# Optimization experiments

Hardware: AMD Instinct MI355X
Metric: run time of the kernel (lower is better)

Reference implementation:

```python
import jax, jax.numpy as jnp
import numpy as np

N = 50000          # n_sample
F = 64             # n_feature
DEG = 16           # edges per node
E = N * DEG
HID = 256          # n_hidden
NCLS = 16          # n_class
NPOOL = 3
K = 2              # propagation steps
ALPHA = 1.0        # Propagation alpha
EPS = 1e-5
NODE_POOL = round(N ** (1.0 / NPOOL))          # 37
N0 = round(N / NODE_POOL)                      # 1351
N1 = round(N0 / NODE_POOL)                     # 37
N2 = round(N1 / NODE_POOL)                     # 1


def setup_inputs():
    key = jax.random.key(0)
    ks = jax.random.split(key, 16)
    x = jax.random.normal(ks[0], (N, F), jnp.float32)
    x_cov = jax.random.uniform(ks[1], (N, F), jnp.float32)
    adj_rows = jnp.asarray(np.repeat(np.arange(N, dtype=np.int32), DEG))  # sorted
    adj_cols = jax.random.randint(ks[2], (E,), 0, N, jnp.int32)
    adj_vals = jax.random.uniform(ks[3], (E,), jnp.float32)
    feature_corr = jax.random.uniform(ks[4], (N2, F), jnp.float32)
    bn_gamma = jnp.ones((F,), jnp.float32)
    bn_beta = jnp.zeros((F,), jnp.float32)
    lin = lambda k, i, o: jax.random.normal(k, (i, o), jnp.float32) * 0.05
    W0 = lin(ks[5], F, HID); C0 = jax.random.normal(ks[6], (N0, HID), jnp.float32) * 0.05
    W1 = lin(ks[7], F, HID); C1 = jax.random.normal(ks[8], (N1, HID), jnp.float32) * 0.05
    W2 = lin(ks[9], F, HID); C2 = jax.random.normal(ks[10], (N2, HID), jnp.float32) * 0.05
    mW1 = lin(ks[11], 2 * F, HID); mb1 = jnp.zeros((HID,), jnp.float32)
    mp1 = jnp.full((1,), 0.25, jnp.float32)
    mW2 = lin(ks[12], HID, HID); mb2 = jnp.zeros((HID,), jnp.float32)
    mp2 = jnp.full((1,), 0.25, jnp.float32)
    mW3 = lin(ks[13], HID, NCLS); mb3 = jnp.zeros((NCLS,), jnp.float32)
    return dict(x=x, x_cov=x_cov, adj_vals=adj_vals, feature_corr=feature_corr,
                bn_gamma=bn_gamma, bn_beta=bn_beta, W0=W0, C0=C0, W1=W1, C1=C1,
                W2=W2, C2=C2, mW1=mW1, mb1=mb1, mp1=mp1, mW2=mW2, mb2=mb2, mp2=mp2,
                mW3=mW3, mb3=mb3, adj_rows=adj_rows, adj_cols=adj_cols)


def _pool(xc, W, C, nc):
    # ClusteringLayer: project, hard-assign to nearest centroid, mean-pool,
    # corr = per-node squared deviation from its cluster mean (input resolution).
    h = xc @ W                                                    # [n_prev, HID]
    d = (h * h).sum(-1, keepdims=True) - 2.0 * (h @ C.T) + (C * C).sum(-1)[None, :]
    a = jnp.argmin(d, axis=1)                                     # [n_prev] cluster ids
    cnt = jax.ops.segment_sum(jnp.ones((xc.shape[0],), xc.dtype), a, num_segments=nc)
    pooled = jax.ops.segment_sum(xc, a, num_segments=nc) / jnp.maximum(cnt, 1.0)[:, None]
    corr = (xc - pooled[a]) ** 2                                  # [n_prev, F]
    return pooled, corr, a


def _forward(x, x_cov, adj_vals, feature_corr, bn_gamma, bn_beta, W0, C0, W1, C1,
             W2, C2, mW1, mb1, mp1, mW2, mb2, mp2, mW3, mb3, adj_rows, adj_cols):
    # BatchNorm1d (batch statistics)
    mu = x.mean(0)
    var = x.var(0)
    x = (x - mu) / jnp.sqrt(var + EPS) * bn_gamma + bn_beta
    x0 = x
    # pooling hierarchy
    p0, corr0, a0 = _pool(x_cov, W0, C0, N0)
    p1, corr1, a1 = _pool(p0, W1, C1, N1)
    p2, corr2, a2 = _pool(p1, W2, C2, N2)
    loss = (corr1.mean(0) + corr2.mean(0)).mean() / (NPOOL - 1)
    # gains: spmm(hard assignment, corr_next) is a gather
    g0 = 2.0 * jax.nn.sigmoid(corr2[a1] - corr1)          # [N0, F]
    g1 = 2.0 * jax.nn.sigmoid(feature_corr[a2] - corr2)   # [N1, F]
    # composed node->level cluster ids (masks[1] = masks[0] @ masks[1])
    cl0 = a0               # [N]
    cl1 = a1[a0]           # [N]
    r, c = adj_rows, adj_cols
    # (M diag(g) M^T)[r,c] = g[cl(r)]^2 * 1[cl(r)==cl(c)], masked to adj pattern
    same0 = (cl0[r] == cl0[c])[:, None]
    same1 = (cl1[r] == cl1[c])[:, None]
    vals = adj_vals[:, None] \
        + jnp.where(same0, (g0 * g0)[cl0[r]], jnp.float32(0)) \
        + jnp.where(same1, (g1 * g1)[cl1[r]], jnp.float32(0))     # [E, F]
    # per-feature sparse row softmax
    m = jax.ops.segment_max(vals, r, num_segments=N)
    ev = jnp.exp(vals - m[r])
    s = jax.ops.segment_sum(ev, r, num_segments=N)
    A = ev / s[r]                                                  # [E, F]
    # k propagation steps: per-feature spmm + alpha * x0 residual
    for _ in range(K):
        x = jax.ops.segment_sum(A * x[c], r, num_segments=N) + ALPHA * x0
    # MLP head with PReLU, log-probabilities
    h = jnp.concatenate([x, x0], axis=1)
    h = h @ mW1 + mb1
    h = jnp.where(h >= 0, h, mp1 * h)
    h = h @ mW2 + mb2
    h = jnp.where(h >= 0, h, mp2 * h)
    logits = h @ mW3 + mb3
    out = jax.nn.log_softmax(logits, axis=1)
    return out, loss


def reference(x, x_cov, adj_vals, feature_corr, bn_gamma, bn_beta, W0, C0, W1, C1,
              W2, C2, mW1, mb1, mp1, mW2, mb2, mp2, mW3, mb3, adj_rows, adj_cols):
    return _forward(x, x_cov, adj_vals, feature_corr, bn_gamma, bn_beta, W0, C0,
                    W1, C1, W2, C2, mW1, mb1, mp1, mW2, mb2, mp2, mW3, mb3,
                    adj_rows, adj_cols)
```

## Files before the change

kernel.cpp:

```cpp
#include <hip/hip_runtime.h>
#include <math.h>

#define N_NODES 50000
#define FEA 64
#define DEG 16
#define HID 256
#define NCLS 16
#define NP0 1351
#define NP0T 1408
#define CTILES 11
#define NP1 37
#define EPSV 1e-5f

__global__ __launch_bounds__(256) void bn_reduce(const float* __restrict__ x,
                                                 float* __restrict__ bnsum, float* __restrict__ bnsq) {
    __shared__ float s1[256], s2[256];
    int tid = threadIdx.x;
    int f = tid & 63, sub = tid >> 6;
    float a = 0.f, b = 0.f;
    for (int r = blockIdx.x * 4 + sub; r < N_NODES; r += gridDim.x * 4) {
        float v = x[r * FEA + f];
        a += v; b += v * v;
    }
    s1[tid] = a; s2[tid] = b;
    __syncthreads();
    if (tid < 64) {
        a = s1[tid] + s1[tid + 64] + s1[tid + 128] + s1[tid + 192];
        b = s2[tid] + s2[tid + 64] + s2[tid + 128] + s2[tid + 192];
        atomicAdd(&bnsum[tid], a);
        atomicAdd(&bnsq[tid], b);
    }
}

__global__ __launch_bounds__(256) void bn_apply(const float* __restrict__ x,
                                                const float* __restrict__ bnsum, const float* __restrict__ bnsq,
                                                const float* __restrict__ gamma, const float* __restrict__ beta,
                                                float* __restrict__ x0) {
    int gid = blockIdx.x * 256 + threadIdx.x;
    if (gid >= N_NODES * FEA) return;
    int f = gid & 63;
    float mu = bnsum[f] * (1.0f / N_NODES);
    float var = bnsq[f] * (1.0f / N_NODES) - mu * mu;
    float sc = gamma[f] / sqrtf(var + EPSV);
    x0[gid] = (x[gid] - mu) * sc + beta[f];
}

__global__ void transpose_W0(const float* __restrict__ W0, float* __restrict__ W0t) {
    int idx = blockIdx.x * 256 + threadIdx.x;
    if (idx < FEA * HID) {
        int f = idx >> 8, h = idx & 255;
        W0t[h * FEA + f] = W0[idx];
    }
}

__global__ __launch_bounds__(64) void compute_G2(const float* __restrict__ W0t, const float* __restrict__ C0,
                                                 float* __restrict__ Gt, float* __restrict__ c0n) {
    int j = blockIdx.x, k = threadIdx.x;
    if (j >= NP0) {
        Gt[k * NP0T + j] = 0.f;
        if (k == 0) c0n[j] = 3.4e38f;
        return;
    }
    const float* c = C0 + j * HID;
    float acc = 0.f;
    for (int m = 0; m < HID; ++m) acc += W0t[m * FEA + k] * c[m];
    Gt[k * NP0T + j] = acc;
    float cn = 0.f;
    for (int m = k; m < HID; m += 64) { float v = c[m]; cn += v * v; }
    for (int off = 32; off; off >>= 1) cn += __shfl_xor(cn, off);
    if (k == 0) c0n[j] = cn;
}

__global__ void cnorm(const float* __restrict__ C, float* __restrict__ cn) {
    int j = blockIdx.x, k = threadIdx.x;
    const float* c = C + j * HID;
    float acc = 0.f;
    for (int m = k; m < HID; m += 64) { float v = c[m]; acc += v * v; }
    for (int off = 32; off; off >>= 1) acc += __shfl_xor(acc, off);
    if (k == 0) cn[j] = acc;
}

__global__ __launch_bounds__(256, 2) void argmin0_gemm8(const float* __restrict__ xcov,
                                                        const float* __restrict__ Gt,
                                                        const float* __restrict__ c0n,
                                                        int* __restrict__ a0) {
    __shared__ char smem[36864 + 33792 + 512];
    float* As = (float*)smem;
    float* Bs = (float*)(smem + 36864);
    float* cs = (float*)(smem + 36864 + 33792);
    int t = threadIdx.x;
    int row0 = blockIdx.x * 128;

    {
        int r = t & 127, half = t >> 7;
        int row = row0 + r;
        int fr = r + 4 * (r >> 5);
        if (row < N_NODES) {
            const float4* xp = (const float4*)(xcov + (size_t)row * FEA + half * 32);
            #pragma unroll
            for (int u = 0; u < 8; ++u) {
                float4 v = xp[u];
                int k = half * 32 + u * 4;
                As[(k+0)*144 + fr] = v.x; As[(k+1)*144 + fr] = v.y;
                As[(k+2)*144 + fr] = v.z; As[(k+3)*144 + fr] = v.w;
            }
        } else {
            #pragma unroll
            for (int u = 0; u < 8; ++u) {
                int k = half * 32 + u * 4;
                As[(k+0)*144+fr] = 0.f; As[(k+1)*144+fr] = 0.f;
                As[(k+2)*144+fr] = 0.f; As[(k+3)*144+fr] = 0.f;
            }
        }
    }

    int tr = t & 15, tc = t >> 4;
    int aoff = 8 * tr + 4 * (tr >> 2);
    int boff = 8 * tc;
    unsigned long long best[8];
    #pragma unroll
    for (int r = 0; r < 8; ++r) best[r] = ~0ull;

    for (int tile = 0; tile < CTILES; ++tile) {
        int j0 = tile * 128;
        __syncthreads();
        {
            int kk = t >> 2, g = t & 3;
            const float* gr = Gt + (size_t)kk * NP0T + j0;
            #pragma unroll
            for (int u = 0; u < 8; ++u) {
                int gi = g + 4 * u;
                float4 v = *(const float4*)(gr + gi * 4);
                *(float4*)(Bs + kk * 132 + gi * 4) = v;
            }
        }
        if (t < 128) cs[t] = c0n[j0 + t];
        __syncthreads();

        float acc[8][8];
        #pragma unroll
        for (int r = 0; r < 8; ++r)
            #pragma unroll
            for (int c = 0; c < 8; ++c) acc[r][c] = 0.f;

        for (int k = 0; k < 64; ++k) {
            float4 av0 = *(const float4*)(As + k * 144 + aoff);
            float4 av1 = *(const float4*)(As + k * 144 + aoff + 4);
            float4 bv0 = *(const float4*)(Bs + k * 132 + boff);
            float4 bv1 = *(const float4*)(Bs + k * 132 + boff + 4);
            float av[8] = {av0.x, av0.y, av0.z, av0.w, av1.x, av1.y, av1.z, av1.w};
            float bv[8] = {bv0.x, bv0.y, bv0.z, bv0.w, bv1.x, bv1.y, bv1.z, bv1.w};
            #pragma unroll
            for (int r = 0; r < 8; ++r)
                #pragma unroll
                for (int c = 0; c < 8; ++c) acc[r][c] += av[r] * bv[c];
        }
        #pragma unroll
        for (int c = 0; c < 8; ++c) {
            int j = j0 + boff + c;
            float cn = cs[boff + c];
            #pragma unroll
            for (int r = 0; r < 8; ++r) {
                float d = cn - 2.0f * acc[r][c];
                unsigned s = __float_as_uint(d);
                unsigned u2 = ((int)s < 0) ? ~s : (s | 0x80000000u);
                unsigned long long p = ((unsigned long long)u2 << 32) | (unsigned)j;
                if (p < best[r]) best[r] = p;
            }
        }
    }

    __syncthreads();
    unsigned long long* pmin = (unsigned long long*)Bs;
    #pragma unroll
    for (int r = 0; r < 8; ++r) pmin[(8 * tr + r) * 16 + tc] = best[r];
    __syncthreads();
    if (t < 128) {
        unsigned long long b = pmin[t * 16];
        #pragma unroll
        for (int q = 1; q < 16; ++q) {
            unsigned long long v = pmin[t * 16 + q];
            if (v < b) b = v;
        }
        int row = row0 + t;
        if (row < N_NODES) a0[row] = (int)(unsigned)b;
    }
}

__global__ __launch_bounds__(256) void hist0(const int* __restrict__ a0, int* __restrict__ hist) {
    int i = blockIdx.x * 256 + threadIdx.x;
    bool act = i < N_NODES;
    int j = act ? a0[i] : -1;
    unsigned long long todo = __ballot(act);
    int lane = threadIdx.x & 63;
    while (todo) {
        int leader = __ffsll((long long)todo) - 1;
        int lj = __shfl(j, leader);
        unsigned long long grp = __ballot(act && j == lj);
        if (lane == leader) atomicAdd(&hist[lj], __popcll(grp));
        todo &= ~grp;
    }
}

__global__ __launch_bounds__(256) void scan0(const int* __restrict__ hist, int* __restrict__ off,
                                             int* __restrict__ cursor) {
    __shared__ int wsum[4];
    int t = threadIdx.x;
    int c0 = t * 6;
    int loc[6]; int s = 0;
    #pragma unroll
    for (int u = 0; u < 6; ++u) {
        int j = c0 + u;
        int h = (j < NP0) ? hist[j] : 0;
        loc[u] = s; s += h;
    }
    int lane = t & 63, w = t >> 6;
    int v = s;
    #pragma unroll
    for (int d = 1; d < 64; d <<= 1) {
        int up = __shfl_up(v, d);
        if (lane >= d) v += up;
    }
    if (lane == 63) wsum[w] = v;
    __syncthreads();
    int woff = 0;
    for (int q = 0; q < w; ++q) woff += wsum[q];
    int excl = woff + v - s;
    #pragma unroll
    for (int u = 0; u < 6; ++u) {
        int j = c0 + u;
        if (j < NP0) { off[j] = excl + loc[u]; cursor[j] = excl + loc[u]; }
    }
    if (t == 255) off[NP0] = excl + s;
}

__global__ __launch_bounds__(256) void scatter0(const int* __restrict__ a0, int* __restrict__ cursor,
                                                int* __restrict__ order, int* __restrict__ csrt) {
    int i = blockIdx.x * 256 + threadIdx.x;
    bool act = i < N_NODES;
    int j = act ? a0[i] : -1;
    int lane = threadIdx.x & 63;
    unsigned long long todo = __ballot(act);
    int pos = 0;
    while (todo) {
        int leader = __ffsll((long long)todo) - 1;
        int lj = __shfl(j, leader);
        unsigned long long grp = __ballot(act && j == lj);
        int base = 0;
        if (lane == leader) base = atomicAdd(&cursor[lj], __popcll(grp));
        base = __shfl(base, leader);
        if (act && j == lj)
            pos = base + __popcll(grp & ((1ull << lane) - 1ull));
        todo &= ~grp;
    }
    if (act) { order[pos] = i; csrt[pos] = j; }
}

__global__ __launch_bounds__(256) void pool0seg(const int* __restrict__ order, const int* __restrict__ csrt,
                                                const float* __restrict__ xcov, double* __restrict__ p0d) {
    int lane = threadIdx.x & 63;
    int w = threadIdx.x >> 6;
    int base = (blockIdx.x * 4 + w) * 16;
    if (base >= N_NODES) return;
    int n = N_NODES - base; if (n > 16) n = 16;
    float vals[16]; int cl[16];
    #pragma unroll
    for (int r = 0; r < 16; ++r) {
        if (r < n) {
            int idx = order[base + r];
            cl[r] = csrt[base + r];
            vals[r] = xcov[(size_t)idx * FEA + lane];
        } else { cl[r] = -1; vals[r] = 0.f; }
    }
    double acc = (double)vals[0]; int cur = cl[0];
    #pragma unroll
    for (int r = 1; r < 16; ++r) {
        if (r < n) {
            if (cl[r] == cur) { acc += (double)vals[r]; }
            else { atomicAdd(&p0d[(size_t)cur * FEA + lane], acc); acc = (double)vals[r]; cur = cl[r]; }
        }
    }
    atomicAdd(&p0d[(size_t)cur * FEA + lane], acc);
}

__global__ void pool_fin0(const double* __restrict__ p0d, const int* __restrict__ hist,
                          float* __restrict__ p0, int total) {
    int gid = blockIdx.x * 256 + threadIdx.x;
    if (gid < total) p0[gid] = (float)(p0d[gid] / (double)max(hist[gid >> 6], 1));
}

__global__ __launch_bounds__(64) void level1(const float* __restrict__ p0, const float* __restrict__ W1,
                                             const float* __restrict__ C1, const float* __restrict__ c1n,
                                             int* __restrict__ a1) {
    int i = blockIdx.x;
    int lane = threadIdx.x;
    const float* pr = p0 + (size_t)i * FEA;
    float h[4] = {0.f, 0.f, 0.f, 0.f};
    for (int k = 0; k < FEA; ++k) {
        float pv = pr[k];
        #pragma unroll
        for (int q = 0; q < 4; ++q) h[q] += pv * W1[k * HID + q * 64 + lane];
    }
    float hh = h[0]*h[0] + h[1]*h[1] + h[2]*h[2] + h[3]*h[3];
    for (int off = 32; off; off >>= 1) hh += __shfl_xor(hh, off);
    float best = 3.4e38f; int bj = 0;
    for (int j = 0; j < NP1; ++j) {
        const float* cj = C1 + j * HID;
        float dp = h[0]*cj[lane] + h[1]*cj[64+lane] + h[2]*cj[128+lane] + h[3]*cj[192+lane];
        for (int off = 32; off; off >>= 1) dp += __shfl_xor(dp, off);
        float d = hh - 2.0f * dp + c1n[j];
        if (d < best) { best = d; bj = j; }
    }
    if (lane == 0) a1[i] = bj;
}

__global__ __launch_bounds__(256) void pool1(const float* __restrict__ p0, const int* __restrict__ a1,
                                             float* __restrict__ p1) {
    __shared__ float s[4][64];
    __shared__ int scnt[4];
    int j = blockIdx.x;
    int lane = threadIdx.x & 63, w = threadIdx.x >> 6;
    float acc = 0.f; int cnt = 0;
    for (int i = w; i < NP0; i += 4) {
        if (a1[i] == j) { acc += p0[i * FEA + lane]; cnt++; }
    }
    s[w][lane] = acc;
    if (lane == 0) scnt[w] = cnt;
    __syncthreads();
    if (w == 0) {
        float tsum = s[0][lane] + s[1][lane] + s[2][lane] + s[3][lane];
        int c = scnt[0] + scnt[1] + scnt[2] + scnt[3];
        p1[j * FEA + lane] = tsum / fmaxf((float)c, 1.0f);
    }
}

__global__ __launch_bounds__(256) void level2(const float* __restrict__ p1, const float* __restrict__ fc,
                                              float* __restrict__ corr2, float* __restrict__ g1sq,
                                              float* __restrict__ loss2f) {
    __shared__ float p2s[64];
    __shared__ float lacc[64];
    int tid = threadIdx.x;
    if (tid < 64) {
        float s = 0.f;
        for (int i = 0; i < NP1; ++i) s += p1[i * FEA + tid];
        p2s[tid] = s * (1.0f / NP1);
        lacc[tid] = 0.f;
    }
    __syncthreads();
    for (int t = tid; t < NP1 * FEA; t += 256) {
        int f = t & 63;
        float dv = p1[t] - p2s[f];
        float c2 = dv * dv;
        corr2[t] = c2;
        float sg = 2.0f / (1.0f + __expf(-(fc[f] - c2)));
        g1sq[t] = sg * sg;
        atomicAdd(&lacc[f], c2);
    }
    __syncthreads();
    if (tid < 64) loss2f[tid] = lacc[tid] * (1.0f / NP1);
}

__global__ __launch_bounds__(256) void corr1_g0(const float* __restrict__ p0, const float* __restrict__ p1,
                                                const int* __restrict__ a1, const float* __restrict__ corr2,
                                                float* __restrict__ g0sq, float* __restrict__ loss1g) {
    __shared__ float sh[256];
    int tid = threadIdx.x;
    int f = tid & 63, sub = tid >> 6;
    int i = blockIdx.x * 4 + sub;
    float c1v = 0.f;
    if (i < NP0) {
        int a = a1[i];
        float dv = p0[i * FEA + f] - p1[a * FEA + f];
        c1v = dv * dv;
        float sg = 2.0f / (1.0f + __expf(-(corr2[a * FEA + f] - c1v)));
        g0sq[i * FEA + f] = sg * sg;
    }
    sh[tid] = c1v;
    __syncthreads();
    if (tid < 64) atomicAdd(&loss1g[tid], sh[tid] + sh[tid+64] + sh[tid+128] + sh[tid+192]);
}

__global__ void loss_final(const float* __restrict__ loss1g, const float* __restrict__ loss2f,
                           float* __restrict__ out_loss) {
    int lane = threadIdx.x;
    float v = loss1g[lane] * (1.0f / NP0) + loss2f[lane];
    for (int off = 32; off; off >>= 1) v += __shfl_xor(v, off);
    if (lane == 0) out_loss[0] = v * (1.0f / FEA) * 0.5f;
}

__global__ void cl1map(const int* __restrict__ a0, const int* __restrict__ a1, int* __restrict__ cl1) {
    int i = blockIdx.x * 256 + threadIdx.x;
    if (i < N_NODES) cl1[i] = a1[a0[i]];
}

__global__ __launch_bounds__(256) void prop(const float* __restrict__ xin, const float* __restrict__ x0,
                                            const int* __restrict__ cols, const float* __restrict__ avals,
                                            const int* __restrict__ cl0, const int* __restrict__ cl1,
                                            const float* __restrict__ g0sq, const float* __restrict__ g1sq,
                                            float* __restrict__ xout) {
    int lane = threadIdx.x & 63;
    int i = blockIdx.x * 4 + __builtin_amdgcn_readfirstlane(threadIdx.x >> 6);
    int s0 = cl0[i], s1 = cl1[i];
    float g0f = g0sq[s0 * FEA + lane];
    float g1f = g1sq[s1 * FEA + lane];
    float x0f = x0[(size_t)i * FEA + lane];
    int ce[DEG]; float v[DEG];
    float m = -3.4e38f;
    #pragma unroll
    for (int e = 0; e < DEG; ++e) {
        int c = cols[i * DEG + e];
        ce[e] = c;
        float val = avals[i * DEG + e];
        if (cl0[c] == s0) val += g0f;
        if (cl1[c] == s1) val += g1f;
        v[e] = val;
        m = fmaxf(m, val);
    }
    float se = 0.f, acc = 0.f;
    #pragma unroll
    for (int e = 0; e < DEG; ++e) {
        float w = __expf(v[e] - m);
        se += w;
        acc += w * xin[(size_t)ce[e] * FEA + lane];
    }
    xout[(size_t)i * FEA + lane] = acc / se + x0f;
}

__global__ __launch_bounds__(256, 2) void gemm_prelu(const float* __restrict__ s0, const float* __restrict__ s1,
                                                     const float* __restrict__ s2, const float* __restrict__ s3,
                                                     int nchunks, int lda,
                                                     const float* __restrict__ W, const float* __restrict__ b,
                                                     const float* __restrict__ pp, float* __restrict__ out) {
    __shared__ float As[64 * 144];
    __shared__ float Bs[64 * 140];
    int t = threadIdx.x;
    int mt = blockIdx.x >> 1, nt = blockIdx.x & 1;
    int row0 = mt * 128, n0 = nt * 128;
    int tr = t & 15, tc = t >> 4;
    int aoff = 8 * tr + 4 * (tr >> 2);
    int boff = 8 * tc + 4 * (tc >> 2);

    float acc[8][8];
    #pragma unroll
    for (int r = 0; r < 8; ++r)
        #pragma unroll
        for (int c = 0; c < 8; ++c) acc[r][c] = 0.f;

    int ar = t & 127, ahalf = t >> 7;
    int arow = row0 + ar;
    int afr = ar + 4 * (ar >> 5);
    int bkk = t >> 2, bpart = t & 3;

    for (int c = 0; c < nchunks; ++c) {
        const float* Ap = (c == 0) ? s0 : (c == 1) ? s1 : (c == 2) ? s2 : s3;
        __syncthreads();
        if (arow < N_NODES) {
            const float4* xp = (const float4*)(Ap + (size_t)arow * lda + ahalf * 32);
            #pragma unroll
            for (int u = 0; u < 8; ++u) {
                float4 v = xp[u];
                int k = ahalf * 32 + u * 4;
                As[(k+0)*144 + afr] = v.x; As[(k+1)*144 + afr] = v.y;
                As[(k+2)*144 + afr] = v.z; As[(k+3)*144 + afr] = v.w;
            }
        } else {
            #pragma unroll
            for (int u = 0; u < 8; ++u) {
                int k = ahalf * 32 + u * 4;
                As[(k+0)*144+afr] = 0.f; As[(k+1)*144+afr] = 0.f;
                As[(k+2)*144+afr] = 0.f; As[(k+3)*144+afr] = 0.f;
            }
        }
        {
            const float* wr = W + (size_t)(c * 64 + bkk) * HID + n0;
            #pragma unroll
            for (int u = 0; u < 8; ++u) {
                int ci = (bpart + 4 * u) * 4;
                float4 v = *(const float4*)(wr + ci);
                int fc = ci + 4 * (ci >> 5);
                *(float4*)(Bs + bkk * 140 + fc) = v;
            }
        }
        __syncthreads();
        for (int k = 0; k < 64; ++k) {
            float4 av0 = *(const float4*)(As + k * 144 + aoff);
            float4 av1 = *(const float4*)(As + k * 144 + aoff + 4);
            float4 bv0 = *(const float4*)(Bs + k * 140 + boff);
            float4 bv1 = *(const float4*)(Bs + k * 140 + boff + 4);
            float av[8] = {av0.x, av0.y, av0.z, av0.w, av1.x, av1.y, av1.z, av1.w};
            float bv[8] = {bv0.x, bv0.y, bv0.z, bv0.w, bv1.x, bv1.y, bv1.z, bv1.w};
            #pragma unroll
            for (int r = 0; r < 8; ++r)
                #pragma unroll
                for (int cc = 0; cc < 8; ++cc) acc[r][cc] += av[r] * bv[cc];
        }
    }
    float p = pp[0];
    float bb[8];
    #pragma unroll
    for (int cc = 0; cc < 8; ++cc) bb[cc] = b[n0 + 8 * tc + cc];
    #pragma unroll
    for (int r = 0; r < 8; ++r) {
        int row = row0 + 8 * tr + r;
        if (row >= N_NODES) break;
        float* o = out + (size_t)row * HID + n0 + 8 * tc;
        float4 o0, o1;
        float h;
        h = acc[r][0] + bb[0]; o0.x = h >= 0.f ? h : p * h;
        h = acc[r][1] + bb[1]; o0.y = h >= 0.f ? h : p * h;
        h = acc[r][2] + bb[2]; o0.z = h >= 0.f ? h : p * h;
        h = acc[r][3] + bb[3]; o0.w = h >= 0.f ? h : p * h;
        h = acc[r][4] + bb[4]; o1.x = h >= 0.f ? h : p * h;
        h = acc[r][5] + bb[5]; o1.y = h >= 0.f ? h : p * h;
        h = acc[r][6] + bb[6]; o1.z = h >= 0.f ? h : p * h;
        h = acc[r][7] + bb[7]; o1.w = h >= 0.f ? h : p * h;
        *(float4*)(o) = o0;
        *(float4*)(o + 4) = o1;
    }
}

__global__ __launch_bounds__(256) void mlp3(const float* __restrict__ hin, const float* __restrict__ W3,
                                            const float* __restrict__ b3, float* __restrict__ out) {
    __shared__ float Ws[HID * NCLS];
    int tid = threadIdx.x;
    for (int t = tid; t < HID * NCLS; t += 256) Ws[t] = W3[t];
    __syncthreads();
    int lane = tid & 63;
    int wv = __builtin_amdgcn_readfirstlane(tid >> 6);
    int rs = lane >> 4, c = lane & 15;
    int row = blockIdx.x * 16 + wv * 4 + rs;
    const float4* hr = (const float4*)(hin + (size_t)row * HID);
    float acc = b3[c];
    for (int k4 = 0; k4 < 64; ++k4) {
        float4 h = hr[k4];
        int k = k4 * 4;
        acc += h.x * Ws[k * NCLS + c];
        acc += h.y * Ws[(k + 1) * NCLS + c];
        acc += h.z * Ws[(k + 2) * NCLS + c];
        acc += h.w * Ws[(k + 3) * NCLS + c];
    }
    float m = acc;
    #pragma unroll
    for (int off = 1; off < 16; off <<= 1) m = fmaxf(m, __shfl_xor(m, off));
    float e = __expf(acc - m);
    float s = e;
    #pragma unroll
    for (int off = 1; off < 16; off <<= 1) s += __shfl_xor(s, off);
    out[(size_t)row * NCLS + c] = acc - m - __logf(s);
}

extern "C" void kernel_launch(void* const* d_in, const int* in_sizes, int n_in,
                              void* d_out, int out_size, void* d_ws, size_t ws_size,
                              hipStream_t stream) {
    const float* x     = (const float*)d_in[0];
    const float* xcov  = (const float*)d_in[1];
    const float* avals = (const float*)d_in[2];
    const float* fc    = (const float*)d_in[3];
    const float* gamma = (const float*)d_in[4];
    const float* beta  = (const float*)d_in[5];
    const float* W0    = (const float*)d_in[6];
    const float* C0    = (const float*)d_in[7];
    const float* W1    = (const float*)d_in[8];
    const float* C1    = (const float*)d_in[9];
    const float* mW1   = (const float*)d_in[12];
    const float* mb1   = (const float*)d_in[13];
    const float* mp1   = (const float*)d_in[14];
    const float* mW2   = (const float*)d_in[15];
    const float* mb2   = (const float*)d_in[16];
    const float* mp2   = (const float*)d_in[17];
    const float* mW3   = (const float*)d_in[18];
    const float* mb3   = (const float*)d_in[19];
    const int* cols    = (const int*)d_in[21];

    float* ws = (float*)d_ws;
    size_t off = 0;
    auto alloc = [&](size_t n) { float* p = ws + off; off += (n + 63) & ~(size_t)63; return p; };

    float* x0    = alloc((size_t)N_NODES * FEA);
    float* h1b   = alloc((size_t)N_NODES * HID);
    float* h2b   = alloc((size_t)N_NODES * HID);
    float* W0t   = alloc(HID * FEA);
    float* Gt    = alloc((size_t)FEA * NP0T);
    float* c0n   = alloc(NP0T);
    float* c1n   = alloc(NP1);
    float* g0sq  = alloc(NP0 * FEA);
    float* g1sq  = alloc(NP1 * FEA);
    float* corr2 = alloc(NP1 * FEA);
    float* loss2f= alloc(64);
    float* p1    = alloc(NP1 * FEA);
    float* p0    = alloc(NP0 * FEA);
    int*   a0    = (int*)alloc(N_NODES);
    int*   cl1   = (int*)alloc(N_NODES);
    int*   a1    = (int*)alloc(NP0);
    int*   order = (int*)alloc(N_NODES);
    int*   csrt  = (int*)alloc(N_NODES);
    int*   offj  = (int*)alloc(NP0 + 1);
    int*   cursor= (int*)alloc(NP0);
    float* zero0 = ws + off;
    float* bnsum = alloc(64);
    float* bnsq  = alloc(64);
    int*   hist  = (int*)alloc(NP0);
    float* loss1g= alloc(64);
    double* p0d  = (double*)alloc((size_t)NP0 * FEA * 2);
    size_t zbytes = (size_t)((ws + off) - zero0) * sizeof(float);

    float* xb1 = h1b;
    float* xb2 = h2b;
    float* outp = (float*)d_out;

    hipMemsetAsync(zero0, 0, zbytes, stream);

    bn_reduce<<<256, 256, 0, stream>>>(x, bnsum, bnsq);
    bn_apply<<<(N_NODES * FEA) / 256, 256, 0, stream>>>(x, bnsum, bnsq, gamma, beta, x0);

    transpose_W0<<<(FEA * HID + 255) / 256, 256, 0, stream>>>(W0, W0t);
    compute_G2<<<NP0T, 64, 0, stream>>>(W0t, C0, Gt, c0n);
    cnorm<<<NP1, 64, 0, stream>>>(C1, c1n);

    argmin0_gemm8<<<(N_NODES + 127) / 128, 256, 0, stream>>>(xcov, Gt, c0n, a0);

    hist0<<<(N_NODES + 255) / 256, 256, 0, stream>>>(a0, hist);
    scan0<<<1, 256, 0, stream>>>(hist, offj, cursor);
    scatter0<<<(N_NODES + 255) / 256, 256, 0, stream>>>(a0, cursor, order, csrt);
    pool0seg<<<(N_NODES + 63) / 64, 256, 0, stream>>>(order, csrt, xcov, p0d);
    pool_fin0<<<(NP0 * FEA + 255) / 256, 256, 0, stream>>>(p0d, hist, p0, NP0 * FEA);

    level1<<<NP0, 64, 0, stream>>>(p0, W1, C1, c1n, a1);
    pool1<<<NP1, 256, 0, stream>>>(p0, a1, p1);

    level2<<<1, 256, 0, stream>>>(p1, fc, corr2, g1sq, loss2f);
    corr1_g0<<<(NP0 + 3) / 4, 256, 0, stream>>>(p0, p1, a1, corr2, g0sq, loss1g);
    loss_final<<<1, 64, 0, stream>>>(loss1g, loss2f, outp + (size_t)N_NODES * NCLS);

    cl1map<<<(N_NODES + 255) / 256, 256, 0, stream>>>(a0, a1, cl1);

    prop<<<N_NODES / 4, 256, 0, stream>>>(x0, x0, cols, avals, a0, cl1, g0sq, g1sq, xb1);
    prop<<<N_NODES / 4, 256, 0, stream>>>(xb1, x0, cols, avals, a0, cl1, g0sq, g1sq, xb2);

    int gemmGrid = ((N_NODES + 127) / 128) * 2;
    gemm_prelu<<<gemmGrid, 256, 0, stream>>>(xb2, x0, nullptr, nullptr, 2, FEA,
                                             mW1, mb1, mp1, h1b);
    gemm_prelu<<<gemmGrid, 256, 0, stream>>>(h1b, h1b + 64, h1b + 128, h1b + 192, 4, HID,
                                             mW2, mb2, mp2, h2b);
    mlp3<<<N_NODES / 16, 256, 0, stream>>>(h2b, mW3, mb3, outp);
}
```

Baseline: 840.0 us.

## Split argmin GEMM over centroid chunks and merge with 64-bit atomicMin

The nearest-centroid argmin kernel now splits the 11 centroid tiles into 4 chunks, each handled by its own block, giving four times as many blocks. Results are merged through a packed (distance, index) 64-bit atomicMin into a new buffer that is first memset to all ones, and the histogram kernel unpacks the index. Shared memory is cut by staging B in two 32-row K halves with a smaller A pitch, which should raise occupancy. In exchange, each chunk reloads the A tile, and the change adds atomics plus an extra memset.

```diff
diff --git a/kernel.cpp b/kernel.cpp
--- a/kernel.cpp
+++ b/kernel.cpp
@@ -80,16 +80,18 @@
     if (k == 0) cn[j] = acc;
 }
 
-__global__ __launch_bounds__(256, 2) void argmin0_gemm8(const float* __restrict__ xcov,
+__global__ __launch_bounds__(256, 2) void argmin0_split(const float* __restrict__ xcov,
                                                         const float* __restrict__ Gt,
                                                         const float* __restrict__ c0n,
-                                                        int* __restrict__ a0) {
-    __shared__ char smem[36864 + 33792 + 512];
-    float* As = (float*)smem;
-    float* Bs = (float*)(smem + 36864);
-    float* cs = (float*)(smem + 36864 + 33792);
+                                                        unsigned long long* __restrict__ amin) {
+    __shared__ float As[64 * 140];
+    __shared__ float Bs[32 * 132];
+    __shared__ float cs[128];
     int t = threadIdx.x;
-    int row0 = blockIdx.x * 128;
+    int row0 = (blockIdx.x >> 2) * 128;
+    int chunk = blockIdx.x & 3;
+    int tile0 = chunk * 3;
+    int tile1 = tile0 + 3; if (tile1 > CTILES) tile1 = CTILES;
 
     {
         int r = t & 127, half = t >> 7;
@@ -101,15 +103,15 @@
             for (int u = 0; u < 8; ++u) {
                 float4 v = xp[u];
                 int k = half * 32 + u * 4;
-                As[(k+0)*144 + fr] = v.x; As[(k+1)*144 + fr] = v.y;
-                As[(k+2)*144 + fr] = v.z; As[(k+3)*144 + fr] = v.w;
+                As[(k+0)*140 + fr] = v.x; As[(k+1)*140 + fr] = v.y;
+                As[(k+2)*140 + fr] = v.z; As[(k+3)*140 + fr] = v.w;
             }
         } else {
             #pragma unroll
             for (int u = 0; u < 8; ++u) {
                 int k = half * 32 + u * 4;
-                As[(k+0)*144+fr] = 0.f; As[(k+1)*144+fr] = 0.f;
-                As[(k+2)*144+fr] = 0.f; As[(k+3)*144+fr] = 0.f;
+                As[(k+0)*140+fr] = 0.f; As[(k+1)*140+fr] = 0.f;
+                As[(k+2)*140+fr] = 0.f; As[(k+3)*140+fr] = 0.f;
             }
         }
     }
@@ -117,43 +119,46 @@
     int tr = t & 15, tc = t >> 4;
     int aoff = 8 * tr + 4 * (tr >> 2);
     int boff = 8 * tc;
+    int bkk = t >> 3, bpart = t & 7;
     unsigned long long best[8];
     #pragma unroll
     for (int r = 0; r < 8; ++r) best[r] = ~0ull;
 
-    for (int tile = 0; tile < CTILES; ++tile) {
+    for (int tile = tile0; tile < tile1; ++tile) {
         int j0 = tile * 128;
-        __syncthreads();
-        {
-            int kk = t >> 2, g = t & 3;
-            const float* gr = Gt + (size_t)kk * NP0T + j0;
-            #pragma unroll
-            for (int u = 0; u < 8; ++u) {
-                int gi = g + 4 * u;
-                float4 v = *(const float4*)(gr + gi * 4);
-                *(float4*)(Bs + kk * 132 + gi * 4) = v;
-            }
-        }
-        if (t < 128) cs[t] = c0n[j0 + t];
-        __syncthreads();
-
         float acc[8][8];
         #pragma unroll
         for (int r = 0; r < 8; ++r)
             #pragma unroll
             for (int c = 0; c < 8; ++c) acc[r][c] = 0.f;
 
-        for (int k = 0; k < 64; ++k) {
-            float4 av0 = *(const float4*)(As + k * 144 + aoff);
-            float4 av1 = *(const float4*)(As + k * 144 + aoff + 4);
-            float4 bv0 = *(const float4*)(Bs + k * 132 + boff);
-            float4 bv1 = *(const float4*)(Bs + k * 132 + boff + 4);
-            float av[8] = {av0.x, av0.y, av0.z, av0.w, av1.x, av1.y, av1.z, av1.w};
-            float bv[8] = {bv0.x, bv0.y, bv0.z, bv0.w, bv1.x, bv1.y, bv1.z, bv1.w};
-            #pragma unroll
-            for (int r = 0; r < 8; ++r)
+        for (int kh = 0; kh < 2; ++kh) {
+            __syncthreads();
+            {
+                const float* gr = Gt + (size_t)(kh * 32 + bkk) * NP0T + j0;
                 #pragma unroll
-                for (int c = 0; c < 8; ++c) acc[r][c] += av[r] * bv[c];
+                for (int u = 0; u < 4; ++u) {
+                    int gi = bpart + 8 * u;
+                    float4 v = *(const float4*)(gr + gi * 4);
+                    *(float4*)(Bs + bkk * 132 + gi * 4) = v;
+                }
+            }
+            if (kh == 0 && t < 128) cs[t] = c0n[j0 + t];
+            __syncthreads();
+            #pragma unroll 4
+            for (int k2 = 0; k2 < 32; ++k2) {
+                int k = kh * 32 + k2;
+                float4 av0 = *(const float4*)(As + k * 140 + aoff);
+                float4 av1 = *(const float4*)(As + k * 140 + aoff + 4);
+                float4 bv0 = *(const float4*)(Bs + k2 * 132 + boff);
+                float4 bv1 = *(const float4*)(Bs + k2 * 132 + boff + 4);
+                float av[8] = {av0.x, av0.y, av0.z, av0.w, av1.x, av1.y, av1.z, av1.w};
+                float bv[8] = {bv0.x, bv0.y, bv0.z, bv0.w, bv1.x, bv1.y, bv1.z, bv1.w};
+                #pragma unroll
+                for (int r = 0; r < 8; ++r)
+                    #pragma unroll
+                    for (int c = 0; c < 8; ++c) acc[r][c] += av[r] * bv[c];
+            }
         }
         #pragma unroll
         for (int c = 0; c < 8; ++c) {
@@ -183,14 +188,16 @@
             if (v < b) b = v;
         }
         int row = row0 + t;
-        if (row < N_NODES) a0[row] = (int)(unsigned)b;
-    }
-}
-
-__global__ __launch_bounds__(256) void hist0(const int* __restrict__ a0, int* __restrict__ hist) {
+        if (row < N_NODES) atomicMin(&amin[row], b);
+    }
+}
+
+__global__ __launch_bounds__(256) void hist0(const unsigned long long* __restrict__ amin,
+                                             int* __restrict__ a0, int* __restrict__ hist) {
     int i = blockIdx.x * 256 + threadIdx.x;
     bool act = i < N_NODES;
-    int j = act ? a0[i] : -1;
+    int j = act ? (int)(unsigned)amin[i] : -1;
+    if (act) a0[i] = j;
     unsigned long long todo = __ballot(act);
     int lane = threadIdx.x & 63;
     while (todo) {
@@ -596,6 +603,7 @@
     int*   csrt  = (int*)alloc(N_NODES);
     int*   offj  = (int*)alloc(NP0 + 1);
     int*   cursor= (int*)alloc(NP0);
+    unsigned long long* amin = (unsigned long long*)alloc((size_t)N_NODES * 2);
     float* zero0 = ws + off;
     float* bnsum = alloc(64);
     float* bnsq  = alloc(64);
@@ -609,6 +617,7 @@
     float* outp = (float*)d_out;
 
     hipMemsetAsync(zero0, 0, zbytes, stream);
+    hipMemsetAsync(amin, 0xFF, (size_t)N_NODES * 8, stream);
 
     bn_reduce<<<256, 256, 0, stream>>>(x, bnsum, bnsq);
     bn_apply<<<(N_NODES * FEA) / 256, 256, 0, stream>>>(x, bnsum, bnsq, gamma, beta, x0);
@@ -617,9 +626,10 @@
     compute_G2<<<NP0T, 64, 0, stream>>>(W0t, C0, Gt, c0n);
     cnorm<<<NP1, 64, 0, stream>>>(C1, c1n);
 
-    argmin0_gemm8<<<(N_NODES + 127) / 128, 256, 0, stream>>>(xcov, Gt, c0n, a0);
-
-    hist0<<<(N_NODES + 255) / 256, 256, 0, stream>>>(a0, hist);
+    int mtiles = (N_NODES + 127) / 128;
+    argmin0_split<<<mtiles * 4, 256, 0, stream>>>(xcov, Gt, c0n, amin);
+
+    hist0<<<(N_NODES + 255) / 256, 256, 0, stream>>>(amin, a0, hist);
     scan0<<<1, 256, 0, stream>>>(hist, offj, cursor);
     scatter0<<<(N_NODES + 255) / 256, 256, 0, stream>>>(a0, cursor, order, csrt);
     pool0seg<<<(N_NODES + 63) / 64, 256, 0, stream>>>(order, csrt, xcov, p0d);
@@ -637,7 +647,7 @@
     prop<<<N_NODES / 4, 256, 0, stream>>>(x0, x0, cols, avals, a0, cl1, g0sq, g1sq, xb1);
     prop<<<N_NODES / 4, 256, 0, stream>>>(xb1, x0, cols, avals, a0, cl1, g0sq, g1sq, xb2);
 
-    int gemmGrid = ((N_NODES + 127) / 128) * 2;
+    int gemmGrid = mtiles * 2;
     gemm_prelu<<<gemmGrid, 256, 0, stream>>>(xb2, x0, nullptr, nullptr, 2, FEA,
                                              mW1, mb1, mp1, h1b);
     gemm_prelu<<<gemmGrid, 256, 0, stream>>>(h1b, h1b + 64, h1b + 128, h1b + 192, 4, HID,
```

New measurement: 843.7 us. Within noise of the previous version (+0.4%).
